# Kernel optimization log

Hardware: AMD Instinct MI355X
Metric: run time of the kernel (lower is better)

Reference implementation:

```python
import jax, jax.numpy as jnp
import numpy as np
import math

DENOM = 32.0

# e3nn scalar_activation normalizes the activation to unit second moment under N(0,1).
# Compute the gelu normalization constant by Gauss-Hermite quadrature.
_zs, _ws = np.polynomial.hermite_e.hermegauss(64)
_g = 0.5 * _zs * (1.0 + np.array([math.erf(z / math.sqrt(2.0)) for z in _zs]))
C_GELU = float(1.0 / math.sqrt((_ws * _g * _g).sum() / math.sqrt(2.0 * math.pi)))


def _spherical_harmonics(r):
    # r: [E,3] unit vectors. Component-normalized real SH for l=1,2,3.
    x, y, z = r[..., 0], r[..., 1], r[..., 2]
    s3, s5, s15 = math.sqrt(3.0), math.sqrt(5.0), math.sqrt(15.0)
    s7, s105 = math.sqrt(7.0), math.sqrt(105.0)
    s35_8, s21_8 = math.sqrt(35.0 / 8.0), math.sqrt(21.0 / 8.0)
    Y1 = s3 * r                                                     # [E,3]
    Y2 = jnp.stack([s15 * x * y, s15 * y * z, 0.5 * s5 * (3 * z * z - 1),
                    s15 * x * z, 0.5 * s15 * (x * x - y * y)], -1)   # [E,5]
    Y3 = jnp.stack([s35_8 * y * (3 * x * x - y * y), s105 * x * y * z,
                    s21_8 * y * (5 * z * z - 1), 0.5 * s7 * z * (5 * z * z - 3),
                    s21_8 * x * (5 * z * z - 1), 0.5 * s105 * z * (x * x - y * y),
                    s35_8 * x * (x * x - 3 * y * y)], -1)            # [E,7]
    return [Y1, Y2, Y3]


def setup_inputs() -> dict:
    key = jax.random.key(0)
    k = jax.random.split(key, 7)
    N, E, MUL, TMUL = 32768, 1048576, 16, 32
    return {
        "x": jax.random.normal(k[0], (N, MUL), jnp.float32),
        "positions": jax.random.normal(k[1], (N, 3), jnp.float32),
        "W_pre": jax.random.normal(k[2], (4, MUL, TMUL), jnp.float32),
        "W_post": jax.random.normal(k[3], (4, TMUL, TMUL), jnp.float32),
        "W_shortcut": jax.random.normal(k[4], (MUL, TMUL), jnp.float32),
        "senders": jax.random.randint(k[5], (E,), 0, N, jnp.int32),
        "receivers": jax.random.randint(k[6], (E,), 0, N, jnp.int32),
    }


def reference(x, positions, W_pre, W_post, W_shortcut, senders, receivers):
    N, mul = x.shape
    tmul = W_pre.shape[-1]
    # --- edge update: sh of relative positions, tensor product with sender scalars ---
    rvec = positions[receivers] - positions[senders]                 # [E,3]
    n = jnp.linalg.norm(rvec, axis=-1, keepdims=True)
    rhat = rvec / jnp.where(n == 0, 1.0, n)
    Ys = _spherical_harmonics(rhat)
    s = x[senders]                                                   # [E,mul] (0e)
    # --- aggregate edge features at receivers (segment sum) ---
    agg = [jax.ops.segment_sum(s, receivers, num_segments=N)]        # 0e block
    for Y in Ys:
        e = (s[:, :, None] * Y[:, None, :]).reshape(s.shape[0], -1)  # 0e x l -> l
        agg.append(jax.ops.segment_sum(e, receivers, num_segments=N).reshape(N, mul, Y.shape[-1]))
    # --- node update: linear_pre -> scalar act -> linear_post, plus shortcut ---
    inv_in = 1.0 / math.sqrt(mul)
    inv_mid = 1.0 / math.sqrt(tmul)
    out = []
    for l in range(4):
        a = agg[l] / DENOM
        if l == 0:
            p = (a @ W_pre[0]) * inv_in
            p = C_GELU * jax.nn.gelu(p, approximate=False)           # act on 0e scalars only
            q = (p @ W_post[0]) * inv_mid
            q = q + (x @ W_shortcut) * inv_in                        # shortcut: only 0e path exists
            out.append(q)
        else:
            p = jnp.einsum('nui,uv->nvi', a, W_pre[l]) * inv_in
            q = jnp.einsum('nvi,vw->nwi', p, W_post[l]) * inv_mid
            out.append(q.reshape(N, -1))
    return jnp.concatenate(out, axis=-1)                              # [N, tmul*16]
```

## Files before the change

### kernel.cpp

```cpp
#include <hip/hip_runtime.h>
#include <math.h>

#define NN 32768
#define EN 1048576
#define NBIN 256
#define BINCAP 8192
#define TILE 4096

#define C_GELU_F 1.5335262f

__global__ __launch_bounds__(512) void bin_k(const int* __restrict__ snd,
                                             const int* __restrict__ rcv,
                                             const float* __restrict__ pos,
                                             float4* __restrict__ posw,
                                             int* __restrict__ bin_cur,
                                             unsigned* __restrict__ binbuf) {
    __shared__ unsigned cnt[NBIN];
    __shared__ unsigned excl[NBIN];
    __shared__ unsigned cur2[NBIN];
    __shared__ unsigned gbase[NBIN];
    __shared__ unsigned stage[TILE];
    int t = threadIdx.x;
    int tile = blockIdx.x * TILE;
    if (t < NBIN) { cnt[t] = 0; cur2[t] = 0; }
    if (t < 128) {
        int n = (blockIdx.x << 7) + t;
        posw[n] = make_float4(pos[3*n], pos[3*n+1], pos[3*n+2], 0.f);
    }
    __syncthreads();

    unsigned w[TILE / 512];
#pragma unroll
    for (int i = 0; i < TILE / 512; ++i) {
        int e = tile + i * 512 + t;
        unsigned r = (unsigned)rcv[e], s = (unsigned)snd[e];
        w[i] = (r << 15) | s;
        atomicAdd(&cnt[w[i] >> 22], 1u);
    }
    __syncthreads();

    unsigned my = (t < NBIN) ? cnt[t] : 0u;
    if (t < NBIN) excl[t] = my;
    __syncthreads();
    for (int d = 1; d < NBIN; d <<= 1) {
        unsigned v = (t < NBIN && t >= d) ? excl[t - d] : 0u;
        __syncthreads();
        if (t < NBIN) excl[t] += v;
        __syncthreads();
    }
    if (t < NBIN) {
        unsigned myexcl = excl[t] - my;
        gbase[t] = atomicAdd((unsigned*)&bin_cur[t], my);
        excl[t] = myexcl;
    }
    __syncthreads();

#pragma unroll
    for (int i = 0; i < TILE / 512; ++i) {
        unsigned b = w[i] >> 22;
        unsigned p = excl[b] + atomicAdd(&cur2[b], 1u);
        stage[p] = w[i];
    }
    __syncthreads();

    for (int p = t; p < TILE; p += 512) {
        unsigned ww = stage[p];
        unsigned b = ww >> 22;
        unsigned idx = gbase[b] + ((unsigned)p - excl[b]);
        if (idx < BINCAP) binbuf[b * BINCAP + idx] = ww;
    }
}

__global__ __launch_bounds__(1024) void csr_k(const int* __restrict__ bin_cur,
                                              const unsigned* __restrict__ binbuf,
                                              int* __restrict__ row_ptr,
                                              int* __restrict__ edge_csr) {
    __shared__ unsigned sc[NBIN];
    __shared__ unsigned cnt[128];
    __shared__ unsigned excl[128];
    __shared__ unsigned cur2[128];
    int b = blockIdx.x;
    int t = threadIdx.x;

    if (t < NBIN) sc[t] = (unsigned)bin_cur[t];
    __syncthreads();
    for (int d = 1; d < NBIN; d <<= 1) {
        unsigned v = (t < NBIN && t >= d) ? sc[t - d] : 0u;
        __syncthreads();
        if (t < NBIN) sc[t] += v;
        __syncthreads();
    }
    int Mraw = bin_cur[b];
    int base = (int)(sc[b] - (unsigned)Mraw);
    int M = Mraw > BINCAP ? BINCAP : Mraw;
    if (t < 128) { cnt[t] = 0; cur2[t] = 0; }
    __syncthreads();

    const unsigned* bb = binbuf + b * BINCAP;
    for (int i = t; i < M; i += 1024)
        atomicAdd(&cnt[(bb[i] >> 15) & 127], 1u);
    __syncthreads();

    if (t < 128) excl[t] = cnt[t];
    __syncthreads();
    for (int d = 1; d < 128; d <<= 1) {
        unsigned v = (t >= d && t < 128) ? excl[t - d] : 0u;
        __syncthreads();
        if (t < 128) excl[t] += v;
        __syncthreads();
    }
    if (t < 128) {
        unsigned e = excl[t] - cnt[t];
        excl[t] = e;
        row_ptr[(b << 7) + t] = base + (int)e;
        if (b == NBIN - 1 && t == 127) row_ptr[NN] = base + (int)(e + cnt[127]);
    }
    __syncthreads();

    for (int i = t; i < M; i += 1024) {
        unsigned ww = bb[i];
        unsigned r7 = (ww >> 15) & 127;
        unsigned dst = excl[r7] + atomicAdd(&cur2[r7], 1u);
        edge_csr[base + dst] = (int)(ww & 0x7FFF);
    }
}

#define GROUPS 32
#define BLK 512
#define YST 20
#define GST (16*YST + 8)

__global__ __launch_bounds__(512, 4) void fused_k(const float* __restrict__ x,
                                                  const float4* __restrict__ posw,
                                                  const int* __restrict__ row_ptr,
                                                  const int* __restrict__ edge_csr,
                                                  const float* __restrict__ Wpre,
                                                  const float* __restrict__ Wpost,
                                                  const float* __restrict__ Wsc,
                                                  float* __restrict__ out) {
    __shared__ float sPre[4*516];
    __shared__ float sPost[4*1028];
    __shared__ float sSc[512];
    __shared__ float sY[GROUPS * GST];

    int t = threadIdx.x;
    for (int idx = t; idx < 2048; idx += BLK)
        sPre[(idx >> 9)*516 + (idx & 511)] = Wpre[idx];
    for (int idx = t; idx < 4096; idx += BLK)
        sPost[(idx >> 10)*1028 + (idx & 1023)] = Wpost[idx];
    sSc[t] = Wsc[t];
    __syncthreads();

    int g = t >> 4;
    int j = t & 15;
    int n = blockIdx.x * GROUPS + g;
    int beg = row_ptr[n], end = row_ptr[n + 1];
    int cnt = end - beg;
    float4 rp = posw[n];
    float* yg = sY + g * GST;

    const float s3   = 1.7320508075688772f;
    const float s5   = 2.2360679774997896f;
    const float s15  = 3.8729833462074170f;
    const float s7   = 2.6457513110645907f;
    const float s105 = 10.246950765959598f;
    const float s35_8 = 2.0916500663351889f;
    const float s21_8 = 1.6201851746019651f;

    float acc[16];
#pragma unroll
    for (int u = 0; u < 16; ++u) acc[u] = 0.f;

    int nch = (cnt + 15) >> 4;
    if (nch > 0) {
        int ki0 = (j < cnt) ? j : cnt - 1;
        int sE = edge_csr[beg + ki0];
        float4 sp = posw[sE];

        for (int c = 0; c < nch; ++c) {
            int kn = ((c + 1) << 4) + j;
            int kiN = (kn < cnt) ? kn : cnt - 1;
            int sEn = edge_csr[beg + kiN];

            float vx = rp.x - sp.x, vy = rp.y - sp.y, vz = rp.z - sp.z;
            float n2 = vx*vx + vy*vy + vz*vz;
            float inv;
            if (n2 > 0.f) {
                inv = rsqrtf(n2);
                inv = inv * (1.5f - 0.5f * n2 * inv * inv);
            } else inv = 0.f;
            float X = vx*inv, Y = vy*inv, Z = vz*inv;
            float XX = X*X, YY = Y*Y, ZZ = Z*Z;
            float m = (((c << 4) + j) < cnt) ? 1.f : 0.f;

            float* yr = yg + j * YST;
            ((float4*)yr)[0] = make_float4(m, m*(s3*X), m*(s3*Y), m*(s3*Z));
            ((float4*)yr)[1] = make_float4(m*(s15*X*Y), m*(s15*Y*Z),
                                           m*(0.5f*s5*(3.f*ZZ - 1.f)), m*(s15*X*Z));
            ((float4*)yr)[2] = make_float4(m*(0.5f*s15*(XX - YY)),
                                           m*(s35_8*Y*(3.f*XX - YY)),
                                           m*(s105*X*Y*Z),
                                           m*(s21_8*Y*(5.f*ZZ - 1.f)));
            ((float4*)yr)[3] = make_float4(m*(0.5f*s7*Z*(5.f*ZZ - 3.f)),
                                           m*(s21_8*X*(5.f*ZZ - 1.f)),
                                           m*(0.5f*s105*Z*(XX - YY)),
                                           m*(s35_8*X*(XX - 3.f*YY)));

            int se[16];
#pragma unroll
            for (int e = 0; e < 16; ++e)
                se[e] = __shfl(sE, (t & 48) + e, 64);
            float yt[16];
#pragma unroll
            for (int e = 0; e < 16; ++e)
                yt[e] = yg[e * YST + j];

            float4 spn = posw[sEn];

#pragma unroll
            for (int e = 0; e < 16; ++e) {
                float y = yt[e];
                const float4* xp = (const float4*)(x + (se[e] << 4));
                float4 a0 = xp[0], a1 = xp[1], a2 = xp[2], a3 = xp[3];
                acc[0]  += a0.x * y;  acc[1]  += a0.y * y;
                acc[2]  += a0.z * y;  acc[3]  += a0.w * y;
                acc[4]  += a1.x * y;  acc[5]  += a1.y * y;
                acc[6]  += a1.z * y;  acc[7]  += a1.w * y;
                acc[8]  += a2.x * y;  acc[9]  += a2.y * y;
                acc[10] += a2.z * y;  acc[11] += a2.w * y;
                acc[12] += a3.x * y;  acc[13] += a3.y * y;
                acc[14] += a3.z * y;  acc[15] += a3.w * y;
            }

            sE = sEn; sp = spn;
        }
    }

    int l, i, offl, deg;
    if (j == 0)      { l = 0; i = 0;     offl = 0;   deg = 1; }
    else if (j < 4)  { l = 1; i = j - 1; offl = 32;  deg = 3; }
    else if (j < 9)  { l = 2; i = j - 4; offl = 128; deg = 5; }
    else             { l = 3; i = j - 9; offl = 288; deg = 7; }

    const float c1 = 0.0078125f;
    const float c2 = 0.17677669529663687f;

    float p[32];
#pragma unroll
    for (int v = 0; v < 32; ++v) p[v] = 0.f;
    const float* wp = sPre + l * 516;
#pragma unroll
    for (int uu = 0; uu < 16; ++uu) {
        float a = acc[uu];
        const float4* w4 = (const float4*)(wp + (uu << 5));
#pragma unroll
        for (int vq = 0; vq < 8; ++vq) {
            float4 w = w4[vq];
            p[4*vq+0] += a * w.x;
            p[4*vq+1] += a * w.y;
            p[4*vq+2] += a * w.z;
            p[4*vq+3] += a * w.w;
        }
    }
#pragma unroll
    for (int v = 0; v < 32; ++v) p[v] *= c1;

    if (j == 0) {
#pragma unroll
        for (int v = 0; v < 32; ++v) {
            float pv = p[v];
            p[v] = C_GELU_F * 0.5f * pv * (1.f + erff(pv * 0.7071067811865476f));
        }
    }

    float q[32];
#pragma unroll
    for (int w = 0; w < 32; ++w) q[w] = 0.f;
    const float* wq = sPost + l * 1028;
#pragma unroll
    for (int v = 0; v < 32; ++v) {
        float pv = p[v];
        const float4* w4 = (const float4*)(wq + (v << 5));
#pragma unroll
        for (int wd = 0; wd < 8; ++wd) {
            float4 w = w4[wd];
            q[4*wd+0] += pv * w.x;
            q[4*wd+1] += pv * w.y;
            q[4*wd+2] += pv * w.z;
            q[4*wd+3] += pv * w.w;
        }
    }
#pragma unroll
    for (int w = 0; w < 32; ++w) q[w] *= c2;

    if (j == 0) {
        const float* xp = x + (n << 4);
#pragma unroll
        for (int uu = 0; uu < 16; ++uu) {
            float xv = 0.25f * xp[uu];
            const float4* w4 = (const float4*)(sSc + (uu << 5));
#pragma unroll
            for (int wd = 0; wd < 8; ++wd) {
                float4 w = w4[wd];
                q[4*wd+0] += xv * w.x;
                q[4*wd+1] += xv * w.y;
                q[4*wd+2] += xv * w.z;
                q[4*wd+3] += xv * w.w;
            }
        }
    }

    float* op = out + (n << 9) + offl + i;
#pragma unroll
    for (int w = 0; w < 32; ++w) op[w * deg] = q[w];
}

extern "C" void kernel_launch(void* const* d_in, const int* in_sizes, int n_in,
                              void* d_out, int out_size, void* d_ws, size_t ws_size,
                              hipStream_t stream) {
    const float* x     = (const float*)d_in[0];
    const float* pos   = (const float*)d_in[1];
    const float* Wpre  = (const float*)d_in[2];
    const float* Wpost = (const float*)d_in[3];
    const float* Wsc   = (const float*)d_in[4];
    const int*   snd   = (const int*)d_in[5];
    const int*   rcv   = (const int*)d_in[6];
    float* out = (float*)d_out;

    char* ws = (char*)d_ws;
    int*      bin_cur   = (int*)(ws);
    int*      row_ptr   = (int*)(ws + 2048);
    float4*   posw      = (float4*)(ws + 0x30000);
    int*      edge_csr  = (int*)(ws + 0xB0000);
    unsigned* binbuf    = (unsigned*)(ws + 0x500000);

    hipMemsetAsync(bin_cur, 0, NBIN * sizeof(int), stream);
    bin_k<<<EN / TILE, 512, 0, stream>>>(snd, rcv, pos, posw, bin_cur, binbuf);
    csr_k<<<NBIN, 1024, 0, stream>>>(bin_cur, binbuf, row_ptr, edge_csr);
    fused_k<<<NN / GROUPS, BLK, 0, stream>>>(x, posw, row_ptr, edge_csr,
                                             Wpre, Wpost, Wsc, out);
}
```

Before: 186.1 us.

## Assign one wavefront per node and split channels across lanes; finer binning

The fused kernel now gives each 64-lane wavefront one node instead of 16 lanes. Each quarter-wave handles 4 of the 16 input channels, and a cross-lane shuffle reduction assembles the pre-linear output. Weights are read straight from global/L1 instead of being staged in shared memory, and each lane computes 8 output channels rather than 32. This cuts register pressure so more waves fit per CU (launch bounds raised to 8). The binning and CSR kernels use twice as many bins, each half the size, with smaller tiles, which adds more blocks but risks overflowing a bin capacity of 4096.

```diff
diff --git a/kernel.cpp b/kernel.cpp
--- a/kernel.cpp
+++ b/kernel.cpp
@@ -3,9 +3,9 @@
 
 #define NN 32768
 #define EN 1048576
-#define NBIN 256
-#define BINCAP 8192
-#define TILE 4096
+#define NBIN 512
+#define BINCAP 4096
+#define TILE 2048
 
 #define C_GELU_F 1.5335262f
 
@@ -22,9 +22,9 @@
     __shared__ unsigned stage[TILE];
     int t = threadIdx.x;
     int tile = blockIdx.x * TILE;
-    if (t < NBIN) { cnt[t] = 0; cur2[t] = 0; }
-    if (t < 128) {
-        int n = (blockIdx.x << 7) + t;
+    cnt[t] = 0; cur2[t] = 0;
+    if (t < 64) {
+        int n = (blockIdx.x << 6) + t;
         posw[n] = make_float4(pos[3*n], pos[3*n+1], pos[3*n+2], 0.f);
     }
     __syncthreads();
@@ -35,20 +35,20 @@
         int e = tile + i * 512 + t;
         unsigned r = (unsigned)rcv[e], s = (unsigned)snd[e];
         w[i] = (r << 15) | s;
-        atomicAdd(&cnt[w[i] >> 22], 1u);
-    }
-    __syncthreads();
-
-    unsigned my = (t < NBIN) ? cnt[t] : 0u;
-    if (t < NBIN) excl[t] = my;
+        atomicAdd(&cnt[w[i] >> 21], 1u);
+    }
+    __syncthreads();
+
+    unsigned my = cnt[t];
+    excl[t] = my;
     __syncthreads();
     for (int d = 1; d < NBIN; d <<= 1) {
-        unsigned v = (t < NBIN && t >= d) ? excl[t - d] : 0u;
-        __syncthreads();
-        if (t < NBIN) excl[t] += v;
-        __syncthreads();
-    }
-    if (t < NBIN) {
+        unsigned v = (t >= d) ? excl[t - d] : 0u;
+        __syncthreads();
+        excl[t] += v;
+        __syncthreads();
+    }
+    {
         unsigned myexcl = excl[t] - my;
         gbase[t] = atomicAdd((unsigned*)&bin_cur[t], my);
         excl[t] = myexcl;
@@ -57,7 +57,7 @@
 
 #pragma unroll
     for (int i = 0; i < TILE / 512; ++i) {
-        unsigned b = w[i] >> 22;
+        unsigned b = w[i] >> 21;
         unsigned p = excl[b] + atomicAdd(&cur2[b], 1u);
         stage[p] = w[i];
     }
@@ -65,72 +65,71 @@
 
     for (int p = t; p < TILE; p += 512) {
         unsigned ww = stage[p];
-        unsigned b = ww >> 22;
+        unsigned b = ww >> 21;
         unsigned idx = gbase[b] + ((unsigned)p - excl[b]);
         if (idx < BINCAP) binbuf[b * BINCAP + idx] = ww;
     }
 }
 
-__global__ __launch_bounds__(1024) void csr_k(const int* __restrict__ bin_cur,
-                                              const unsigned* __restrict__ binbuf,
-                                              int* __restrict__ row_ptr,
-                                              int* __restrict__ edge_csr) {
+__global__ __launch_bounds__(512) void csr_k(const int* __restrict__ bin_cur,
+                                             const unsigned* __restrict__ binbuf,
+                                             int* __restrict__ row_ptr,
+                                             int* __restrict__ edge_csr) {
     __shared__ unsigned sc[NBIN];
-    __shared__ unsigned cnt[128];
-    __shared__ unsigned excl[128];
-    __shared__ unsigned cur2[128];
+    __shared__ unsigned cnt[64];
+    __shared__ unsigned excl[64];
+    __shared__ unsigned cur2[64];
     int b = blockIdx.x;
     int t = threadIdx.x;
 
-    if (t < NBIN) sc[t] = (unsigned)bin_cur[t];
+    sc[t] = (unsigned)bin_cur[t];
     __syncthreads();
     for (int d = 1; d < NBIN; d <<= 1) {
-        unsigned v = (t < NBIN && t >= d) ? sc[t - d] : 0u;
-        __syncthreads();
-        if (t < NBIN) sc[t] += v;
+        unsigned v = (t >= d) ? sc[t - d] : 0u;
+        __syncthreads();
+        sc[t] += v;
         __syncthreads();
     }
     int Mraw = bin_cur[b];
     int base = (int)(sc[b] - (unsigned)Mraw);
     int M = Mraw > BINCAP ? BINCAP : Mraw;
-    if (t < 128) { cnt[t] = 0; cur2[t] = 0; }
+    if (t < 64) { cnt[t] = 0; cur2[t] = 0; }
     __syncthreads();
 
     const unsigned* bb = binbuf + b * BINCAP;
-    for (int i = t; i < M; i += 1024)
-        atomicAdd(&cnt[(bb[i] >> 15) & 127], 1u);
-    __syncthreads();
-
-    if (t < 128) excl[t] = cnt[t];
-    __syncthreads();
-    for (int d = 1; d < 128; d <<= 1) {
-        unsigned v = (t >= d && t < 128) ? excl[t - d] : 0u;
-        __syncthreads();
-        if (t < 128) excl[t] += v;
-        __syncthreads();
-    }
-    if (t < 128) {
+    for (int i = t; i < M; i += 512)
+        atomicAdd(&cnt[(bb[i] >> 15) & 63], 1u);
+    __syncthreads();
+
+    if (t < 64) excl[t] = cnt[t];
+    __syncthreads();
+    for (int d = 1; d < 64; d <<= 1) {
+        unsigned v = (t >= d && t < 64) ? excl[t - d] : 0u;
+        __syncthreads();
+        if (t < 64) excl[t] += v;
+        __syncthreads();
+    }
+    if (t < 64) {
         unsigned e = excl[t] - cnt[t];
         excl[t] = e;
-        row_ptr[(b << 7) + t] = base + (int)e;
-        if (b == NBIN - 1 && t == 127) row_ptr[NN] = base + (int)(e + cnt[127]);
-    }
-    __syncthreads();
-
-    for (int i = t; i < M; i += 1024) {
+        row_ptr[(b << 6) + t] = base + (int)e;
+        if (b == NBIN - 1 && t == 63) row_ptr[NN] = base + (int)(e + cnt[63]);
+    }
+    __syncthreads();
+
+    for (int i = t; i < M; i += 512) {
         unsigned ww = bb[i];
-        unsigned r7 = (ww >> 15) & 127;
-        unsigned dst = excl[r7] + atomicAdd(&cur2[r7], 1u);
+        unsigned r6 = (ww >> 15) & 63;
+        unsigned dst = excl[r6] + atomicAdd(&cur2[r6], 1u);
         edge_csr[base + dst] = (int)(ww & 0x7FFF);
     }
 }
 
-#define GROUPS 32
 #define BLK 512
 #define YST 20
-#define GST (16*YST + 8)
-
-__global__ __launch_bounds__(512, 4) void fused_k(const float* __restrict__ x,
+#define WROW (64 * YST)
+
+__global__ __launch_bounds__(512, 8) void fused_k(const float* __restrict__ x,
                                                   const float4* __restrict__ posw,
                                                   const int* __restrict__ row_ptr,
                                                   const int* __restrict__ edge_csr,
@@ -138,26 +137,18 @@
                                                   const float* __restrict__ Wpost,
                                                   const float* __restrict__ Wsc,
                                                   float* __restrict__ out) {
-    __shared__ float sPre[4*516];
-    __shared__ float sPost[4*1028];
-    __shared__ float sSc[512];
-    __shared__ float sY[GROUPS * GST];
+    __shared__ float sY[8 * WROW];
 
     int t = threadIdx.x;
-    for (int idx = t; idx < 2048; idx += BLK)
-        sPre[(idx >> 9)*516 + (idx & 511)] = Wpre[idx];
-    for (int idx = t; idx < 4096; idx += BLK)
-        sPost[(idx >> 10)*1028 + (idx & 1023)] = Wpost[idx];
-    sSc[t] = Wsc[t];
-    __syncthreads();
-
-    int g = t >> 4;
-    int j = t & 15;
-    int n = blockIdx.x * GROUPS + g;
+    int wv = t >> 6;
+    int lane = t & 63;
+    int h = lane >> 4;
+    int j = lane & 15;
+    int n = (blockIdx.x << 3) + wv;
     int beg = row_ptr[n], end = row_ptr[n + 1];
     int cnt = end - beg;
     float4 rp = posw[n];
-    float* yg = sY + g * GST;
+    float* yg = sY + wv * WROW;
 
     const float s3   = 1.7320508075688772f;
     const float s5   = 2.2360679774997896f;
@@ -167,72 +158,49 @@
     const float s35_8 = 2.0916500663351889f;
     const float s21_8 = 1.6201851746019651f;
 
-    float acc[16];
-#pragma unroll
-    for (int u = 0; u < 16; ++u) acc[u] = 0.f;
-
-    int nch = (cnt + 15) >> 4;
-    if (nch > 0) {
-        int ki0 = (j < cnt) ? j : cnt - 1;
-        int sE = edge_csr[beg + ki0];
+    float acc0 = 0.f, acc1 = 0.f, acc2 = 0.f, acc3 = 0.f;
+    const float* xh = x + (h << 2);
+
+    int nch = (cnt + 63) >> 6;
+    for (int c = 0; c < nch; ++c) {
+        int k = (c << 6) + lane;
+        int ki = k < cnt ? k : cnt - 1;
+        int sE = edge_csr[beg + ki];
         float4 sp = posw[sE];
 
-        for (int c = 0; c < nch; ++c) {
-            int kn = ((c + 1) << 4) + j;
-            int kiN = (kn < cnt) ? kn : cnt - 1;
-            int sEn = edge_csr[beg + kiN];
-
-            float vx = rp.x - sp.x, vy = rp.y - sp.y, vz = rp.z - sp.z;
-            float n2 = vx*vx + vy*vy + vz*vz;
-            float inv;
-            if (n2 > 0.f) {
-                inv = rsqrtf(n2);
-                inv = inv * (1.5f - 0.5f * n2 * inv * inv);
-            } else inv = 0.f;
-            float X = vx*inv, Y = vy*inv, Z = vz*inv;
-            float XX = X*X, YY = Y*Y, ZZ = Z*Z;
-            float m = (((c << 4) + j) < cnt) ? 1.f : 0.f;
-
-            float* yr = yg + j * YST;
-            ((float4*)yr)[0] = make_float4(m, m*(s3*X), m*(s3*Y), m*(s3*Z));
-            ((float4*)yr)[1] = make_float4(m*(s15*X*Y), m*(s15*Y*Z),
-                                           m*(0.5f*s5*(3.f*ZZ - 1.f)), m*(s15*X*Z));
-            ((float4*)yr)[2] = make_float4(m*(0.5f*s15*(XX - YY)),
-                                           m*(s35_8*Y*(3.f*XX - YY)),
-                                           m*(s105*X*Y*Z),
-                                           m*(s21_8*Y*(5.f*ZZ - 1.f)));
-            ((float4*)yr)[3] = make_float4(m*(0.5f*s7*Z*(5.f*ZZ - 3.f)),
-                                           m*(s21_8*X*(5.f*ZZ - 1.f)),
-                                           m*(0.5f*s105*Z*(XX - YY)),
-                                           m*(s35_8*X*(XX - 3.f*YY)));
-
-            int se[16];
-#pragma unroll
-            for (int e = 0; e < 16; ++e)
-                se[e] = __shfl(sE, (t & 48) + e, 64);
-            float yt[16];
-#pragma unroll
-            for (int e = 0; e < 16; ++e)
-                yt[e] = yg[e * YST + j];
-
-            float4 spn = posw[sEn];
-
-#pragma unroll
-            for (int e = 0; e < 16; ++e) {
-                float y = yt[e];
-                const float4* xp = (const float4*)(x + (se[e] << 4));
-                float4 a0 = xp[0], a1 = xp[1], a2 = xp[2], a3 = xp[3];
-                acc[0]  += a0.x * y;  acc[1]  += a0.y * y;
-                acc[2]  += a0.z * y;  acc[3]  += a0.w * y;
-                acc[4]  += a1.x * y;  acc[5]  += a1.y * y;
-                acc[6]  += a1.z * y;  acc[7]  += a1.w * y;
-                acc[8]  += a2.x * y;  acc[9]  += a2.y * y;
-                acc[10] += a2.z * y;  acc[11] += a2.w * y;
-                acc[12] += a3.x * y;  acc[13] += a3.y * y;
-                acc[14] += a3.z * y;  acc[15] += a3.w * y;
-            }
-
-            sE = sEn; sp = spn;
+        float vx = rp.x - sp.x, vy = rp.y - sp.y, vz = rp.z - sp.z;
+        float n2 = vx*vx + vy*vy + vz*vz;
+        float inv;
+        if (n2 > 0.f) {
+            inv = rsqrtf(n2);
+            inv = inv * (1.5f - 0.5f * n2 * inv * inv);
+        } else inv = 0.f;
+        float X = vx*inv, Y = vy*inv, Z = vz*inv;
+        float XX = X*X, YY = Y*Y, ZZ = Z*Z;
+        float m = (k < cnt) ? 1.f : 0.f;
+
+        float* yr = yg + lane * YST;
+        ((float4*)yr)[0] = make_float4(m, m*(s3*X), m*(s3*Y), m*(s3*Z));
+        ((float4*)yr)[1] = make_float4(m*(s15*X*Y), m*(s15*Y*Z),
+                                       m*(0.5f*s5*(3.f*ZZ - 1.f)), m*(s15*X*Z));
+        ((float4*)yr)[2] = make_float4(m*(0.5f*s15*(XX - YY)),
+                                       m*(s35_8*Y*(3.f*XX - YY)),
+                                       m*(s105*X*Y*Z),
+                                       m*(s21_8*Y*(5.f*ZZ - 1.f)));
+        ((float4*)yr)[3] = make_float4(m*(0.5f*s7*Z*(5.f*ZZ - 3.f)),
+                                       m*(s21_8*X*(5.f*ZZ - 1.f)),
+                                       m*(0.5f*s105*Z*(XX - YY)),
+                                       m*(s35_8*X*(XX - 3.f*YY)));
+
+        int rem = cnt - (c << 6); if (rem > 64) rem = 64;
+#pragma unroll 4
+        for (int e = 0; e < rem; ++e) {
+            int se = __shfl(sE, e, 64);
+            float y = yg[e * YST + j];
+            const float4* xp = (const float4*)(xh + (se << 4));
+            float4 a = *xp;
+            acc0 += a.x * y; acc1 += a.y * y;
+            acc2 += a.z * y; acc3 += a.w * y;
         }
     }
 
@@ -248,11 +216,11 @@
     float p[32];
 #pragma unroll
     for (int v = 0; v < 32; ++v) p[v] = 0.f;
-    const float* wp = sPre + l * 516;
-#pragma unroll
-    for (int uu = 0; uu < 16; ++uu) {
-        float a = acc[uu];
-        const float4* w4 = (const float4*)(wp + (uu << 5));
+    const float* wp = Wpre + ((l * 16 + (h << 2)) << 5);
+#pragma unroll
+    for (int u = 0; u < 4; ++u) {
+        float a = (u == 0) ? acc0 : (u == 1) ? acc1 : (u == 2) ? acc2 : acc3;
+        const float4* w4 = (const float4*)(wp + (u << 5));
 #pragma unroll
         for (int vq = 0; vq < 8; ++vq) {
             float4 w = w4[vq];
@@ -263,56 +231,65 @@
         }
     }
 #pragma unroll
+    for (int v = 0; v < 32; ++v) p[v] += __shfl_xor(p[v], 16, 64);
+#pragma unroll
+    for (int v = 0; v < 32; ++v) p[v] += __shfl_xor(p[v], 32, 64);
+#pragma unroll
     for (int v = 0; v < 32; ++v) p[v] *= c1;
 
+    if (lane == 0) {
+#pragma unroll
+        for (int k8 = 0; k8 < 8; ++k8)
+            ((float4*)yg)[k8] = make_float4(p[4*k8], p[4*k8+1], p[4*k8+2], p[4*k8+3]);
+    }
+    if (lane < 32) {
+        float tv = yg[lane];
+        tv = C_GELU_F * 0.5f * tv * (1.f + erff(tv * 0.7071067811865476f));
+        yg[lane] = tv;
+    }
     if (j == 0) {
 #pragma unroll
-        for (int v = 0; v < 32; ++v) {
-            float pv = p[v];
-            p[v] = C_GELU_F * 0.5f * pv * (1.f + erff(pv * 0.7071067811865476f));
+        for (int k8 = 0; k8 < 8; ++k8) {
+            float4 g = ((const float4*)yg)[k8];
+            p[4*k8] = g.x; p[4*k8+1] = g.y; p[4*k8+2] = g.z; p[4*k8+3] = g.w;
         }
     }
 
-    float q[32];
-#pragma unroll
-    for (int w = 0; w < 32; ++w) q[w] = 0.f;
-    const float* wq = sPost + l * 1028;
+    float q[8];
+#pragma unroll
+    for (int w8 = 0; w8 < 8; ++w8) q[w8] = 0.f;
+    const float* wq = Wpost + (l << 10) + (h << 3);
 #pragma unroll
     for (int v = 0; v < 32; ++v) {
         float pv = p[v];
         const float4* w4 = (const float4*)(wq + (v << 5));
-#pragma unroll
-        for (int wd = 0; wd < 8; ++wd) {
-            float4 w = w4[wd];
-            q[4*wd+0] += pv * w.x;
-            q[4*wd+1] += pv * w.y;
-            q[4*wd+2] += pv * w.z;
-            q[4*wd+3] += pv * w.w;
+        float4 wa = w4[0], wb = w4[1];
+        q[0] += pv * wa.x; q[1] += pv * wa.y;
+        q[2] += pv * wa.z; q[3] += pv * wa.w;
+        q[4] += pv * wb.x; q[5] += pv * wb.y;
+        q[6] += pv * wb.z; q[7] += pv * wb.w;
+    }
+#pragma unroll
+    for (int w8 = 0; w8 < 8; ++w8) q[w8] *= c2;
+
+    if (j == 0) {
+        const float* xr = x + (n << 4);
+        const float* ws = Wsc + (h << 3);
+#pragma unroll
+        for (int u = 0; u < 16; ++u) {
+            float xv = 0.25f * xr[u];
+            const float4* w4 = (const float4*)(ws + (u << 5));
+            float4 wa = w4[0], wb = w4[1];
+            q[0] += xv * wa.x; q[1] += xv * wa.y;
+            q[2] += xv * wa.z; q[3] += xv * wa.w;
+            q[4] += xv * wb.x; q[5] += xv * wb.y;
+            q[6] += xv * wb.z; q[7] += xv * wb.w;
         }
     }
-#pragma unroll
-    for (int w = 0; w < 32; ++w) q[w] *= c2;
-
-    if (j == 0) {
-        const float* xp = x + (n << 4);
-#pragma unroll
-        for (int uu = 0; uu < 16; ++uu) {
-            float xv = 0.25f * xp[uu];
-            const float4* w4 = (const float4*)(sSc + (uu << 5));
-#pragma unroll
-            for (int wd = 0; wd < 8; ++wd) {
-                float4 w = w4[wd];
-                q[4*wd+0] += xv * w.x;
-                q[4*wd+1] += xv * w.y;
-                q[4*wd+2] += xv * w.z;
-                q[4*wd+3] += xv * w.w;
-            }
-        }
-    }
-
-    float* op = out + (n << 9) + offl + i;
-#pragma unroll
-    for (int w = 0; w < 32; ++w) op[w * deg] = q[w];
+
+    float* op = out + (n << 9) + offl + i + ((h << 3) * deg);
+#pragma unroll
+    for (int w8 = 0; w8 < 8; ++w8) op[w8 * deg] = q[w8];
 }
 
 extern "C" void kernel_launch(void* const* d_in, const int* in_sizes, int n_in,
@@ -336,7 +313,7 @@
 
     hipMemsetAsync(bin_cur, 0, NBIN * sizeof(int), stream);
     bin_k<<<EN / TILE, 512, 0, stream>>>(snd, rcv, pos, posw, bin_cur, binbuf);
-    csr_k<<<NBIN, 1024, 0, stream>>>(bin_cur, binbuf, row_ptr, edge_csr);
-    fused_k<<<NN / GROUPS, BLK, 0, stream>>>(x, posw, row_ptr, edge_csr,
-                                             Wpre, Wpost, Wsc, out);
+    csr_k<<<NBIN, 512, 0, stream>>>(bin_cur, binbuf, row_ptr, edge_csr);
+    fused_k<<<NN / 8, BLK, 0, stream>>>(x, posw, row_ptr, edge_csr,
+                                        Wpre, Wpost, Wsc, out);
 }
```

Result: slower. 346.6 us (+86.2%).

## Use finer receiver bins and spread GELU across all lanes via shared memory

Applied to the files above, without the earlier changes.

The binning stage now uses 512 bins of 64 nodes with smaller tiles and per-bin capacity, so there are twice as many bin_k and csr_k blocks with 512 threads each. This is meant to improve occupancy and load balance in the CSR build. The GELU on the l=0 path, previously evaluated only by the j==0 threads, is now staged through shared memory so every lane computes erf for two elements, removing the divergent serial erff loop. This assumes the shared-memory layout and the implicit synchronisation between the write, compute and read-back phases are correct. BINCAP also drops to 4096, which gives less headroom before edges in an overfull bin are dropped.

```diff
diff --git a/kernel.cpp b/kernel.cpp
--- a/kernel.cpp
+++ b/kernel.cpp
@@ -3,9 +3,9 @@
 
 #define NN 32768
 #define EN 1048576
-#define NBIN 256
-#define BINCAP 8192
-#define TILE 4096
+#define NBIN 512
+#define BINCAP 4096
+#define TILE 2048
 
 #define C_GELU_F 1.5335262f
 
@@ -22,9 +22,9 @@
     __shared__ unsigned stage[TILE];
     int t = threadIdx.x;
     int tile = blockIdx.x * TILE;
-    if (t < NBIN) { cnt[t] = 0; cur2[t] = 0; }
-    if (t < 128) {
-        int n = (blockIdx.x << 7) + t;
+    cnt[t] = 0; cur2[t] = 0;
+    if (t < 64) {
+        int n = (blockIdx.x << 6) + t;
         posw[n] = make_float4(pos[3*n], pos[3*n+1], pos[3*n+2], 0.f);
     }
     __syncthreads();
@@ -35,20 +35,20 @@
         int e = tile + i * 512 + t;
         unsigned r = (unsigned)rcv[e], s = (unsigned)snd[e];
         w[i] = (r << 15) | s;
-        atomicAdd(&cnt[w[i] >> 22], 1u);
-    }
-    __syncthreads();
-
-    unsigned my = (t < NBIN) ? cnt[t] : 0u;
-    if (t < NBIN) excl[t] = my;
+        atomicAdd(&cnt[w[i] >> 21], 1u);
+    }
+    __syncthreads();
+
+    unsigned my = cnt[t];
+    excl[t] = my;
     __syncthreads();
     for (int d = 1; d < NBIN; d <<= 1) {
-        unsigned v = (t < NBIN && t >= d) ? excl[t - d] : 0u;
-        __syncthreads();
-        if (t < NBIN) excl[t] += v;
-        __syncthreads();
-    }
-    if (t < NBIN) {
+        unsigned v = (t >= d) ? excl[t - d] : 0u;
+        __syncthreads();
+        excl[t] += v;
+        __syncthreads();
+    }
+    {
         unsigned myexcl = excl[t] - my;
         gbase[t] = atomicAdd((unsigned*)&bin_cur[t], my);
         excl[t] = myexcl;
@@ -57,7 +57,7 @@
 
 #pragma unroll
     for (int i = 0; i < TILE / 512; ++i) {
-        unsigned b = w[i] >> 22;
+        unsigned b = w[i] >> 21;
         unsigned p = excl[b] + atomicAdd(&cur2[b], 1u);
         stage[p] = w[i];
     }
@@ -65,62 +65,62 @@
 
     for (int p = t; p < TILE; p += 512) {
         unsigned ww = stage[p];
-        unsigned b = ww >> 22;
+        unsigned b = ww >> 21;
         unsigned idx = gbase[b] + ((unsigned)p - excl[b]);
         if (idx < BINCAP) binbuf[b * BINCAP + idx] = ww;
     }
 }
 
-__global__ __launch_bounds__(1024) void csr_k(const int* __restrict__ bin_cur,
-                                              const unsigned* __restrict__ binbuf,
-                                              int* __restrict__ row_ptr,
-                                              int* __restrict__ edge_csr) {
+__global__ __launch_bounds__(512) void csr_k(const int* __restrict__ bin_cur,
+                                             const unsigned* __restrict__ binbuf,
+                                             int* __restrict__ row_ptr,
+                                             int* __restrict__ edge_csr) {
     __shared__ unsigned sc[NBIN];
-    __shared__ unsigned cnt[128];
-    __shared__ unsigned excl[128];
-    __shared__ unsigned cur2[128];
+    __shared__ unsigned cnt[64];
+    __shared__ unsigned excl[64];
+    __shared__ unsigned cur2[64];
     int b = blockIdx.x;
     int t = threadIdx.x;
 
-    if (t < NBIN) sc[t] = (unsigned)bin_cur[t];
+    sc[t] = (unsigned)bin_cur[t];
     __syncthreads();
     for (int d = 1; d < NBIN; d <<= 1) {
-        unsigned v = (t < NBIN && t >= d) ? sc[t - d] : 0u;
-        __syncthreads();
-        if (t < NBIN) sc[t] += v;
+        unsigned v = (t >= d) ? sc[t - d] : 0u;
+        __syncthreads();
+        sc[t] += v;
         __syncthreads();
     }
     int Mraw = bin_cur[b];
     int base = (int)(sc[b] - (unsigned)Mraw);
     int M = Mraw > BINCAP ? BINCAP : Mraw;
-    if (t < 128) { cnt[t] = 0; cur2[t] = 0; }
+    if (t < 64) { cnt[t] = 0; cur2[t] = 0; }
     __syncthreads();
 
     const unsigned* bb = binbuf + b * BINCAP;
-    for (int i = t; i < M; i += 1024)
-        atomicAdd(&cnt[(bb[i] >> 15) & 127], 1u);
-    __syncthreads();
-
-    if (t < 128) excl[t] = cnt[t];
-    __syncthreads();
-    for (int d = 1; d < 128; d <<= 1) {
-        unsigned v = (t >= d && t < 128) ? excl[t - d] : 0u;
-        __syncthreads();
-        if (t < 128) excl[t] += v;
-        __syncthreads();
-    }
-    if (t < 128) {
+    for (int i = t; i < M; i += 512)
+        atomicAdd(&cnt[(bb[i] >> 15) & 63], 1u);
+    __syncthreads();
+
+    if (t < 64) excl[t] = cnt[t];
+    __syncthreads();
+    for (int d = 1; d < 64; d <<= 1) {
+        unsigned v = (t >= d && t < 64) ? excl[t - d] : 0u;
+        __syncthreads();
+        if (t < 64) excl[t] += v;
+        __syncthreads();
+    }
+    if (t < 64) {
         unsigned e = excl[t] - cnt[t];
         excl[t] = e;
-        row_ptr[(b << 7) + t] = base + (int)e;
-        if (b == NBIN - 1 && t == 127) row_ptr[NN] = base + (int)(e + cnt[127]);
-    }
-    __syncthreads();
-
-    for (int i = t; i < M; i += 1024) {
+        row_ptr[(b << 6) + t] = base + (int)e;
+        if (b == NBIN - 1 && t == 63) row_ptr[NN] = base + (int)(e + cnt[63]);
+    }
+    __syncthreads();
+
+    for (int i = t; i < M; i += 512) {
         unsigned ww = bb[i];
-        unsigned r7 = (ww >> 15) & 127;
-        unsigned dst = excl[r7] + atomicAdd(&cur2[r7], 1u);
+        unsigned r6 = (ww >> 15) & 63;
+        unsigned dst = excl[r6] + atomicAdd(&cur2[r6], 1u);
         edge_csr[base + dst] = (int)(ww & 0x7FFF);
     }
 }
@@ -265,11 +265,32 @@
 #pragma unroll
     for (int v = 0; v < 32; ++v) p[v] *= c1;
 
-    if (j == 0) {
-#pragma unroll
-        for (int v = 0; v < 32; ++v) {
-            float pv = p[v];
-            p[v] = C_GELU_F * 0.5f * pv * (1.f + erff(pv * 0.7071067811865476f));
+    {
+        int lane = t & 63;
+        int gw4 = (t >> 6) << 2;
+        if (j == 0) {
+            float* pg = sY + g * GST;
+#pragma unroll
+            for (int k8 = 0; k8 < 8; ++k8)
+                ((float4*)pg)[k8] = make_float4(p[4*k8], p[4*k8+1],
+                                                p[4*k8+2], p[4*k8+3]);
+        }
+#pragma unroll
+        for (int pass = 0; pass < 2; ++pass) {
+            int idx = (pass << 6) + lane;
+            float* ad = sY + (gw4 + (idx >> 5)) * GST + (idx & 31);
+            float tv = *ad;
+            tv = C_GELU_F * 0.5f * tv * (1.f + erff(tv * 0.7071067811865476f));
+            *ad = tv;
+        }
+        if (j == 0) {
+            float* pg = sY + g * GST;
+#pragma unroll
+            for (int k8 = 0; k8 < 8; ++k8) {
+                float4 gg = ((const float4*)pg)[k8];
+                p[4*k8]   = gg.x; p[4*k8+1] = gg.y;
+                p[4*k8+2] = gg.z; p[4*k8+3] = gg.w;
+            }
         }
     }
 
@@ -336,7 +357,7 @@
 
     hipMemsetAsync(bin_cur, 0, NBIN * sizeof(int), stream);
     bin_k<<<EN / TILE, 512, 0, stream>>>(snd, rcv, pos, posw, bin_cur, binbuf);
-    csr_k<<<NBIN, 1024, 0, stream>>>(bin_cur, binbuf, row_ptr, edge_csr);
+    csr_k<<<NBIN, 512, 0, stream>>>(bin_cur, binbuf, row_ptr, edge_csr);
     fused_k<<<NN / GROUPS, BLK, 0, stream>>>(x, posw, row_ptr, edge_csr,
                                              Wpre, Wpost, Wsc, out);
 }
```

Measured after the change: 194.7 us. 4.6% more time.

## Drop Wpost LDS copy, spread GELU across wave lanes, halve bin tile

Applied to the files above, without the earlier changes.

The post-weight matrix is no longer staged in shared memory and is instead read directly from global (cached) memory, which shrinks the LDS footprint so more blocks can be resident. The exact-erf GELU, previously run serially on one lane per 16-lane group, is now spread across all 64 lanes of a wave through a shared-memory scratch round trip, removing divergence. The binning kernel tile is halved so more blocks run. The trade-offs are global/L1 loads for the weights in the hot loop and extra LDS traffic; the GELU path also relies on wave-synchronous execution without a barrier.

```diff
diff --git a/kernel.cpp b/kernel.cpp
--- a/kernel.cpp
+++ b/kernel.cpp
@@ -5,7 +5,7 @@
 #define EN 1048576
 #define NBIN 256
 #define BINCAP 8192
-#define TILE 4096
+#define TILE 2048
 
 #define C_GELU_F 1.5335262f
 
@@ -23,8 +23,8 @@
     int t = threadIdx.x;
     int tile = blockIdx.x * TILE;
     if (t < NBIN) { cnt[t] = 0; cur2[t] = 0; }
-    if (t < 128) {
-        int n = (blockIdx.x << 7) + t;
+    if (t < 64) {
+        int n = (blockIdx.x << 6) + t;
         posw[n] = make_float4(pos[3*n], pos[3*n+1], pos[3*n+2], 0.f);
     }
     __syncthreads();
@@ -139,15 +139,12 @@
                                                   const float* __restrict__ Wsc,
                                                   float* __restrict__ out) {
     __shared__ float sPre[4*516];
-    __shared__ float sPost[4*1028];
     __shared__ float sSc[512];
     __shared__ float sY[GROUPS * GST];
 
     int t = threadIdx.x;
     for (int idx = t; idx < 2048; idx += BLK)
         sPre[(idx >> 9)*516 + (idx & 511)] = Wpre[idx];
-    for (int idx = t; idx < 4096; idx += BLK)
-        sPost[(idx >> 10)*1028 + (idx & 1023)] = Wpost[idx];
     sSc[t] = Wsc[t];
     __syncthreads();
 
@@ -265,18 +262,39 @@
 #pragma unroll
     for (int v = 0; v < 32; ++v) p[v] *= c1;
 
-    if (j == 0) {
-#pragma unroll
-        for (int v = 0; v < 32; ++v) {
-            float pv = p[v];
-            p[v] = C_GELU_F * 0.5f * pv * (1.f + erff(pv * 0.7071067811865476f));
+    {
+        int lane = t & 63;
+        int gw4 = (t >> 6) << 2;
+        if (j == 0) {
+            float* pg = sY + g * GST;
+#pragma unroll
+            for (int k8 = 0; k8 < 8; ++k8)
+                ((float4*)pg)[k8] = make_float4(p[4*k8], p[4*k8+1],
+                                                p[4*k8+2], p[4*k8+3]);
+        }
+#pragma unroll
+        for (int pass = 0; pass < 2; ++pass) {
+            int idx = (pass << 6) + lane;
+            float* ad = sY + (gw4 + (idx >> 5)) * GST + (idx & 31);
+            float tv = *ad;
+            tv = C_GELU_F * 0.5f * tv * (1.f + erff(tv * 0.7071067811865476f));
+            *ad = tv;
+        }
+        if (j == 0) {
+            float* pg = sY + g * GST;
+#pragma unroll
+            for (int k8 = 0; k8 < 8; ++k8) {
+                float4 gg = ((const float4*)pg)[k8];
+                p[4*k8]   = gg.x; p[4*k8+1] = gg.y;
+                p[4*k8+2] = gg.z; p[4*k8+3] = gg.w;
+            }
         }
     }
 
     float q[32];
 #pragma unroll
     for (int w = 0; w < 32; ++w) q[w] = 0.f;
-    const float* wq = sPost + l * 1028;
+    const float* wq = Wpost + (l << 10);
 #pragma unroll
     for (int v = 0; v < 32; ++v) {
         float pv = p[v];
```

Measured after the change: 260.9 us. 1.4x slower.
